# Kernel tuning notes

Hardware: AMD Instinct MI355X
Metric: run time of the kernel (lower is better)

## Reference

```python
import jax, jax.numpy as jnp
import numpy as np

DIM = 128

def setup_inputs() -> dict:
    key = jax.random.key(0)
    ks = jax.random.split(key, 4)
    N, C, L = 64, DIM, 4096
    scale = 1.0 / np.sqrt(DIM)
    return {
        "x": jax.random.normal(ks[0], (N, C, L), dtype=jnp.float32),
        "Wq": jax.random.normal(ks[1], (DIM, DIM), dtype=jnp.float32) * scale,
        "bq": jnp.zeros((DIM,), dtype=jnp.float32),
        "Wk": jax.random.normal(ks[2], (DIM, DIM), dtype=jnp.float32) * scale,
        "bk": jnp.zeros((DIM,), dtype=jnp.float32),
        "Wv": jax.random.normal(ks[3], (DIM, DIM), dtype=jnp.float32) * scale,
        "bv": jnp.zeros((DIM,), dtype=jnp.float32),
    }

def reference(x, Wq, bq, Wk, bk, Wv, bv):
    # x: [N, C, L] -> rearrange to [N, L, C]
    h = jnp.transpose(x, (0, 2, 1))                       # [N, L, C]
    q = jnp.einsum('nlc,cd->nld', h, Wq) + bq             # [N, L, D]
    k = jnp.einsum('nlc,cd->nld', h, Wk) + bk             # [N, L, D]
    v = jnp.einsum('nlc,cd->nld', h, Wv) + bv             # [N, L, D]
    # AFT-Simple: softmax over sequence axis of K, global weighted pool of V
    w = jax.nn.softmax(k, axis=1)                         # [N, L, D]
    pooled = jnp.sum(w * v, axis=1, keepdims=True)        # [N, 1, D]
    out = jax.nn.sigmoid(q) * pooled                      # [N, L, D]
    return jnp.transpose(out, (0, 2, 1))                  # [N, C, L]
```

## Files before the change

kernel.cpp:

```cpp
#include <hip/hip_runtime.h>
#include <hip/hip_bf16.h>

#define NB 64
#define CD 128
#define LL 4096
#define LCHUNK 64
#define NCHUNK 64
#define NBG 16
#define CPB 4

typedef __attribute__((ext_vector_type(8))) short short8;
typedef __attribute__((ext_vector_type(4))) float f32x4;
typedef __attribute__((ext_vector_type(2))) unsigned u32x2;
typedef __attribute__((ext_vector_type(4))) unsigned u32x4;

#define LOG2E 1.4426950408889634f

#define WT_OFF   0
#define WSS_OFF  (1u<<20)
#define WSP_OFF  ((1u<<20) + NB*NBG*CD*4)
#define POOL_OFF ((1u<<20) + 2u*NB*NBG*CD*4)
#define WSQ_OFF  (8u<<20)

__device__ __forceinline__ unsigned short f2bf(float f) {
    union { float f; unsigned u; } v; v.f = f;
    unsigned r = v.u + 0x7FFFu + ((v.u >> 16) & 1u);
    return (unsigned short)(r >> 16);
}
__device__ __forceinline__ float bf2f(unsigned short h) {
    union { unsigned u; float f; } v; v.u = ((unsigned)h) << 16;
    return v.f;
}
__device__ __forceinline__ unsigned pack2(float lo, float hi) {
    union { __hip_bfloat162 h; unsigned u; } v;
    v.h = __float22bfloat162_rn(float2{lo, hi});
    return v.u;
}

__global__ void prep_wt(const float* __restrict__ Wq, const float* __restrict__ Wk,
                        const float* __restrict__ Wv, unsigned short* __restrict__ wt) {
    int t = blockIdx.x >> 7;
    int d = blockIdx.x & 127;
    const float* W = (t == 0) ? Wq : (t == 1) ? Wk : Wv;
    int c = threadIdx.x;
    wt[((size_t)t*CD + d)*CD + c] = f2bf(W[c*CD + d]);
}

__global__ __launch_bounds__(1024) __attribute__((amdgpu_waves_per_eu(4, 4)))
void aft_qkv(const float* __restrict__ x, const unsigned short* __restrict__ wt,
             const float* __restrict__ bq, const float* __restrict__ bk,
             const float* __restrict__ bv,
             float* __restrict__ wsS, float* __restrict__ wsP,
             unsigned short* __restrict__ wsq) {
    __shared__ char lds[98304 + 17408];
    char* lds_w = lds;
    char* lds_x = lds + 98304;
    const int tid = threadIdx.x;
    const int n = blockIdx.x >> 4;
    const int bg = blockIdx.x & 15;
    const int ww = tid >> 6, lane = tid & 63, r = lane & 15, g = lane >> 4;
    const int dgi = ww & 7, lh = ww >> 3;
    const int d = 16*dgi + r;

#pragma unroll
    for (int k = 0; k < 6; ++k) {
        int bi = tid + 1024*k;
        u32x4 v = *(const u32x4*)((const char*)wt + (size_t)bi*16);
        *(u32x4*)(lds_w + 256*(bi >> 4) + 16*((bi & 15) ^ ((bi >> 4) & 7))) = v;
    }

    const float bql = bq[d], bkl = bk[d], bvl = bv[d];
    float s_run = 0.f, p_run = 0.f;

#pragma unroll 1
    for (int t = 0; t < CPB; ++t) {
        const int l0 = (bg*CPB + t) * LCHUNK;
        __syncthreads();
        {
            const int f = tid & 15, cp = tid >> 4;
            f32x4 lo = *(const f32x4*)(x + ((size_t)n*CD + 2*cp    )*LL + l0 + 4*f);
            f32x4 hi = *(const f32x4*)(x + ((size_t)n*CD + 2*cp + 1)*LL + l0 + 4*f);
            char* base = lds_x + (4*f)*272 + 16*((cp >> 2) ^ (f & 7)) + 4*(cp & 3);
#pragma unroll
            for (int j = 0; j < 4; ++j)
                *(unsigned*)(base + j*272) = pack2(lo[j], hi[j]);
        }
        __syncthreads();

        f32x4 aq[2], ak[2], av[2];
#pragma unroll
        for (int j = 0; j < 2; ++j) {
            aq[j] = (f32x4){0,0,0,0};
            ak[j] = (f32x4){0,0,0,0};
            av[j] = (f32x4){0,0,0,0};
        }
#pragma unroll
        for (int s = 0; s < 4; ++s) {
            const int wb = 16*((4*s + g) ^ (r & 7));
            short8 wqf = *(const short8*)(lds_w +         256*d + wb);
            short8 wkf = *(const short8*)(lds_w + 32768 + 256*d + wb);
            short8 wvf = *(const short8*)(lds_w + 65536 + 256*d + wb);
#pragma unroll
            for (int j = 0; j < 2; ++j) {
                const int lrow = 16*(2*lh + j) + r;
                short8 a = *(const short8*)(lds_x + 272*lrow + 16*((4*s + g) ^ ((lrow >> 2) & 7)));
                aq[j] = __builtin_amdgcn_mfma_f32_16x16x32_bf16(a, wqf, aq[j], 0,0,0);
                ak[j] = __builtin_amdgcn_mfma_f32_16x16x32_bf16(a, wkf, ak[j], 0,0,0);
                av[j] = __builtin_amdgcn_mfma_f32_16x16x32_bf16(a, wvf, av[j], 0,0,0);
            }
        }
#pragma unroll
        for (int j = 0; j < 2; ++j) {
            float sg[4];
#pragma unroll
            for (int v = 0; v < 4; ++v) {
                float e = __builtin_amdgcn_exp2f((ak[j][v] + bkl) * LOG2E);
                s_run += e;
                p_run += e * (av[j][v] + bvl);
                float q2 = (aq[j][v] + bql) * LOG2E;
                sg[v] = __builtin_amdgcn_rcpf(1.f + __builtin_amdgcn_exp2f(-q2));
            }
            u32x2 val = { pack2(sg[0], sg[1]), pack2(sg[2], sg[3]) };
            *(u32x2*)(wsq + ((size_t)n*CD + d)*LL + l0 + 16*(2*lh + j) + 4*g) = val;
        }
    }

    __syncthreads();
    float* redS = (float*)(lds + 98304);
    float* redP = redS + 16*CD;
    s_run += __shfl_xor(s_run, 16, 64);  p_run += __shfl_xor(p_run, 16, 64);
    s_run += __shfl_xor(s_run, 32, 64);  p_run += __shfl_xor(p_run, 32, 64);
    if (g == 0) {
        redS[ww*CD + d] = s_run;
        redP[ww*CD + d] = p_run;
    }
    __syncthreads();
    if (tid < CD) {
        int w0 = tid >> 4;
        float s = redS[w0*CD + tid] + redS[(w0 + 8)*CD + tid];
        float p = redP[w0*CD + tid] + redP[(w0 + 8)*CD + tid];
        size_t idx = ((size_t)n*NBG + bg)*CD + tid;
        wsS[idx] = s;
        wsP[idx] = p;
    }
}

__global__ void aft_pass2(const float* __restrict__ wsS, const float* __restrict__ wsP,
                          float* __restrict__ pooled) {
    int n = blockIdx.x, d = threadIdx.x;
    float s = 0.f, p = 0.f;
    for (int b = 0; b < NBG; ++b) {
        size_t idx = ((size_t)n*NBG + b)*CD + d;
        s += wsS[idx];
        p += wsP[idx];
    }
    pooled[(size_t)n*CD + d] = p / s;
}

__global__ __launch_bounds__(256)
void aft_pass3(const unsigned short* __restrict__ wsq, const float* __restrict__ pooled,
               float* __restrict__ out) {
    const int b = blockIdx.x;
    const int n = b >> 8;
    const int d = (b >> 1) & 127;
    const int half = b & 1;
    const float pl = pooled[(size_t)n*CD + d];
    const size_t base = ((size_t)n*CD + d)*LL + half*2048 + threadIdx.x*8;
    short8 v = *(const short8*)(wsq + base);
    f32x4 o0, o1;
#pragma unroll
    for (int j = 0; j < 4; ++j) {
        o0[j] = bf2f((unsigned short)v[j]) * pl;
        o1[j] = bf2f((unsigned short)v[4+j]) * pl;
    }
    *(f32x4*)(out + base) = o0;
    *(f32x4*)(out + base + 4) = o1;
}

extern "C" void kernel_launch(void* const* d_in, const int* in_sizes, int n_in,
                              void* d_out, int out_size, void* d_ws, size_t ws_size,
                              hipStream_t stream) {
    const float* x  = (const float*)d_in[0];
    const float* Wq = (const float*)d_in[1];
    const float* bq = (const float*)d_in[2];
    const float* Wk = (const float*)d_in[3];
    const float* bk = (const float*)d_in[4];
    const float* Wv = (const float*)d_in[5];
    const float* bv = (const float*)d_in[6];
    float* out = (float*)d_out;
    char* ws = (char*)d_ws;
    unsigned short* wt = (unsigned short*)(ws + WT_OFF);
    float* wsS = (float*)(ws + WSS_OFF);
    float* wsP = (float*)(ws + WSP_OFF);
    float* pooled = (float*)(ws + POOL_OFF);
    unsigned short* wsq = (unsigned short*)(ws + WSQ_OFF);

    prep_wt<<<384, 128, 0, stream>>>(Wq, Wk, Wv, wt);
    aft_qkv<<<NB * NBG, 1024, 0, stream>>>(x, wt, bq, bk, bv, wsS, wsP, wsq);
    aft_pass2<<<NB, CD, 0, stream>>>(wsS, wsP, pooled);
    aft_pass3<<<NB * CD * 2, 256, 0, stream>>>(wsq, pooled, out);
}
```

Before: 109.6 us.

## Double-buffer x staging with prefetch and switch to 32x32 MFMA tiles

The QKV kernel now uses 512-thread blocks that each process 8 chunks instead of 4, halving the grid so the per-block weight load into LDS is amortized over more work. The x tile for the next chunk is prefetched into registers with inline asm loads and written to a second LDS buffer, which removes one barrier per iteration and overlaps global loads with MFMA work. The MFMA tiling moves from 16x16x32 to 32x32x16, cutting LDS fragment loads per output. Risks are fewer blocks (512) giving lower occupancy and CU coverage, and higher register pressure from the 16-wide accumulators.

New measurement: 102.5 us. -6.5%, faster.

```diff
diff --git a/kernel.cpp b/kernel.cpp
--- a/kernel.cpp
+++ b/kernel.cpp
@@ -6,11 +6,12 @@
 #define LL 4096
 #define LCHUNK 64
 #define NCHUNK 64
-#define NBG 16
-#define CPB 4
+#define NBG 8
+#define CPB 8
 
 typedef __attribute__((ext_vector_type(8))) short short8;
 typedef __attribute__((ext_vector_type(4))) float f32x4;
+typedef __attribute__((ext_vector_type(16))) float f32x16;
 typedef __attribute__((ext_vector_type(2))) unsigned u32x2;
 typedef __attribute__((ext_vector_type(4))) unsigned u32x4;
 
@@ -35,6 +36,12 @@
     union { __hip_bfloat162 h; unsigned u; } v;
     v.h = __float22bfloat162_rn(float2{lo, hi});
     return v.u;
+}
+__device__ __forceinline__ f32x4 gload16f(const float* p) {
+    f32x4 d;
+    asm volatile("global_load_dwordx4 %0, %1, off"
+                 : "=&v"(d) : "v"((unsigned long long)(uintptr_t)p));
+    return d;
 }
 
 __global__ void prep_wt(const float* __restrict__ Wq, const float* __restrict__ Wk,
@@ -46,102 +53,114 @@
     wt[((size_t)t*CD + d)*CD + c] = f2bf(W[c*CD + d]);
 }
 
-__global__ __launch_bounds__(1024) __attribute__((amdgpu_waves_per_eu(4, 4)))
+__device__ __forceinline__ void stage_x_write(char* bufx, int f, int cp, f32x4 lo, f32x4 hi) {
+    char* base = bufx + (4*f)*272 + 16*((cp >> 2) ^ (f & 7)) + 4*(cp & 3);
+#pragma unroll
+    for (int j = 0; j < 4; ++j)
+        *(unsigned*)(base + j*272) = pack2(lo[j], hi[j]);
+}
+
+__global__ __launch_bounds__(512)
 void aft_qkv(const float* __restrict__ x, const unsigned short* __restrict__ wt,
              const float* __restrict__ bq, const float* __restrict__ bk,
              const float* __restrict__ bv,
              float* __restrict__ wsS, float* __restrict__ wsP,
              unsigned short* __restrict__ wsq) {
-    __shared__ char lds[98304 + 17408];
-    char* lds_w = lds;
-    char* lds_x = lds + 98304;
+    __shared__ char lds_w[98304];
+    __shared__ char lds_x[2][17408];
+    __shared__ float red_s[4][32];
+    __shared__ float red_p[4][32];
     const int tid = threadIdx.x;
-    const int n = blockIdx.x >> 4;
-    const int bg = blockIdx.x & 15;
-    const int ww = tid >> 6, lane = tid & 63, r = lane & 15, g = lane >> 4;
-    const int dgi = ww & 7, lh = ww >> 3;
-    const int d = 16*dgi + r;
-
-#pragma unroll
-    for (int k = 0; k < 6; ++k) {
-        int bi = tid + 1024*k;
+    const int n = blockIdx.x >> 3;
+    const int bg = blockIdx.x & 7;
+    const int ww = tid >> 6, lane = tid & 63;
+    const int u = lane & 31, h = lane >> 5;
+    const int lh = ww & 1, ng = ww >> 1;
+    const int d = 32*ng + u;
+    const int f = tid & 15, tg = tid >> 4;
+
+#pragma unroll
+    for (int k = 0; k < 12; ++k) {
+        int bi = tid + 512*k;
         u32x4 v = *(const u32x4*)((const char*)wt + (size_t)bi*16);
         *(u32x4*)(lds_w + 256*(bi >> 4) + 16*((bi & 15) ^ ((bi >> 4) & 7))) = v;
     }
-
+    {
+        const int l0 = bg*CPB*LCHUNK;
+#pragma unroll
+        for (int it = 0; it < 2; ++it) {
+            int cp = tg + 32*it;
+            f32x4 lo = *(const f32x4*)(x + ((size_t)n*CD + 2*cp    )*LL + l0 + 4*f);
+            f32x4 hi = *(const f32x4*)(x + ((size_t)n*CD + 2*cp + 1)*LL + l0 + 4*f);
+            stage_x_write(lds_x[0], f, cp, lo, hi);
+        }
+    }
     const float bql = bq[d], bkl = bk[d], bvl = bv[d];
     float s_run = 0.f, p_run = 0.f;
+    __syncthreads();
 
 #pragma unroll 1
     for (int t = 0; t < CPB; ++t) {
         const int l0 = (bg*CPB + t) * LCHUNK;
-        __syncthreads();
-        {
-            const int f = tid & 15, cp = tid >> 4;
-            f32x4 lo = *(const f32x4*)(x + ((size_t)n*CD + 2*cp    )*LL + l0 + 4*f);
-            f32x4 hi = *(const f32x4*)(x + ((size_t)n*CD + 2*cp + 1)*LL + l0 + 4*f);
-            char* base = lds_x + (4*f)*272 + 16*((cp >> 2) ^ (f & 7)) + 4*(cp & 3);
-#pragma unroll
-            for (int j = 0; j < 4; ++j)
-                *(unsigned*)(base + j*272) = pack2(lo[j], hi[j]);
-        }
-        __syncthreads();
-
-        f32x4 aq[2], ak[2], av[2];
-#pragma unroll
-        for (int j = 0; j < 2; ++j) {
-            aq[j] = (f32x4){0,0,0,0};
-            ak[j] = (f32x4){0,0,0,0};
-            av[j] = (f32x4){0,0,0,0};
-        }
-#pragma unroll
-        for (int s = 0; s < 4; ++s) {
-            const int wb = 16*((4*s + g) ^ (r & 7));
-            short8 wqf = *(const short8*)(lds_w +         256*d + wb);
-            short8 wkf = *(const short8*)(lds_w + 32768 + 256*d + wb);
-            short8 wvf = *(const short8*)(lds_w + 65536 + 256*d + wb);
-#pragma unroll
-            for (int j = 0; j < 2; ++j) {
-                const int lrow = 16*(2*lh + j) + r;
-                short8 a = *(const short8*)(lds_x + 272*lrow + 16*((4*s + g) ^ ((lrow >> 2) & 7)));
-                aq[j] = __builtin_amdgcn_mfma_f32_16x16x32_bf16(a, wqf, aq[j], 0,0,0);
-                ak[j] = __builtin_amdgcn_mfma_f32_16x16x32_bf16(a, wkf, ak[j], 0,0,0);
-                av[j] = __builtin_amdgcn_mfma_f32_16x16x32_bf16(a, wvf, av[j], 0,0,0);
-            }
-        }
-#pragma unroll
-        for (int j = 0; j < 2; ++j) {
+        f32x4 pf0, pf1, pf2, pf3;
+        if (t + 1 < CPB) {
+            const float* xb = x + (size_t)n*CD*LL + (l0 + LCHUNK) + 4*f;
+            pf0 = gload16f(xb + (size_t)(2*tg     )*LL);
+            pf1 = gload16f(xb + (size_t)(2*tg + 1 )*LL);
+            pf2 = gload16f(xb + (size_t)(2*(tg+32)    )*LL);
+            pf3 = gload16f(xb + (size_t)(2*(tg+32) + 1)*LL);
+        }
+        const char* abase = lds_x[t & 1] + 272*(32*lh + u);
+        const int asw = ((32*lh + u) >> 2) & 7;
+        const char* wb = lds_w + 256*d;
+        const int dsw = d & 7;
+        f32x16 aq = {0,0,0,0,0,0,0,0,0,0,0,0,0,0,0,0};
+        f32x16 ak = {0,0,0,0,0,0,0,0,0,0,0,0,0,0,0,0};
+        f32x16 av = {0,0,0,0,0,0,0,0,0,0,0,0,0,0,0,0};
+#pragma unroll
+        for (int kk = 0; kk < 8; ++kk) {
+            const int cb = 2*kk + h;
+            short8 a   = *(const short8*)(abase + 16*(cb ^ asw));
+            short8 wqf = *(const short8*)(wb           + 16*(cb ^ dsw));
+            short8 wkf = *(const short8*)(wb + 32768   + 16*(cb ^ dsw));
+            short8 wvf = *(const short8*)(wb + 65536   + 16*(cb ^ dsw));
+            aq = __builtin_amdgcn_mfma_f32_32x32x16_bf16(a, wqf, aq, 0,0,0);
+            ak = __builtin_amdgcn_mfma_f32_32x32x16_bf16(a, wkf, ak, 0,0,0);
+            av = __builtin_amdgcn_mfma_f32_32x32x16_bf16(a, wvf, av, 0,0,0);
+        }
+#pragma unroll
+        for (int grp = 0; grp < 4; ++grp) {
             float sg[4];
 #pragma unroll
-            for (int v = 0; v < 4; ++v) {
-                float e = __builtin_amdgcn_exp2f((ak[j][v] + bkl) * LOG2E);
-                s_run += e;
-                p_run += e * (av[j][v] + bvl);
-                float q2 = (aq[j][v] + bql) * LOG2E;
-                sg[v] = __builtin_amdgcn_rcpf(1.f + __builtin_amdgcn_exp2f(-q2));
+            for (int e = 0; e < 4; ++e) {
+                const int reg = 4*grp + e;
+                float ex = __builtin_amdgcn_exp2f((ak[reg] + bkl) * LOG2E);
+                s_run += ex;
+                p_run += ex * (av[reg] + bvl);
+                float q2 = (aq[reg] + bql) * LOG2E;
+                sg[e] = __builtin_amdgcn_rcpf(1.f + __builtin_amdgcn_exp2f(-q2));
             }
             u32x2 val = { pack2(sg[0], sg[1]), pack2(sg[2], sg[3]) };
-            *(u32x2*)(wsq + ((size_t)n*CD + d)*LL + l0 + 16*(2*lh + j) + 4*g) = val;
-        }
-    }
-
+            *(u32x2*)(wsq + ((size_t)n*CD + d)*LL + l0 + 32*lh + 8*grp + 4*h) = val;
+        }
+        if (t + 1 < CPB) {
+            asm volatile("s_waitcnt vmcnt(0)" ::: "memory");
+            __builtin_amdgcn_sched_barrier(0);
+            char* nb = lds_x[(t + 1) & 1];
+            stage_x_write(nb, f, tg,      pf0, pf1);
+            stage_x_write(nb, f, tg + 32, pf2, pf3);
+        }
+        __syncthreads();
+    }
+
+    s_run += __shfl_xor(s_run, 32, 64);
+    p_run += __shfl_xor(p_run, 32, 64);
+    if (lh == 1 && h == 0) { red_s[ng][u] = s_run; red_p[ng][u] = p_run; }
     __syncthreads();
-    float* redS = (float*)(lds + 98304);
-    float* redP = redS + 16*CD;
-    s_run += __shfl_xor(s_run, 16, 64);  p_run += __shfl_xor(p_run, 16, 64);
-    s_run += __shfl_xor(s_run, 32, 64);  p_run += __shfl_xor(p_run, 32, 64);
-    if (g == 0) {
-        redS[ww*CD + d] = s_run;
-        redP[ww*CD + d] = p_run;
-    }
-    __syncthreads();
-    if (tid < CD) {
-        int w0 = tid >> 4;
-        float s = redS[w0*CD + tid] + redS[(w0 + 8)*CD + tid];
-        float p = redP[w0*CD + tid] + redP[(w0 + 8)*CD + tid];
-        size_t idx = ((size_t)n*NBG + bg)*CD + tid;
-        wsS[idx] = s;
-        wsP[idx] = p;
+    if (lh == 0 && h == 0) {
+        size_t idx = ((size_t)n*NBG + bg)*CD + d;
+        wsS[idx] = s_run + red_s[ng][u];
+        wsP[idx] = p_run + red_p[ng][u];
     }
 }
 
@@ -196,7 +215,7 @@
     unsigned short* wsq = (unsigned short*)(ws + WSQ_OFF);
 
     prep_wt<<<384, 128, 0, stream>>>(Wq, Wk, Wv, wt);
-    aft_qkv<<<NB * NBG, 1024, 0, stream>>>(x, wt, bq, bk, bv, wsS, wsP, wsq);
+    aft_qkv<<<NB * NBG, 512, 0, stream>>>(x, wt, bq, bk, bv, wsS, wsP, wsq);
     aft_pass2<<<NB, CD, 0, stream>>>(wsS, wsP, pooled);
     aft_pass3<<<NB * CD * 2, 256, 0, stream>>>(wsq, pooled, out);
 }
```
